# Kernel optimization log

Hardware: AMD Instinct MI355X
Metric: run time of the kernel (lower is better)

The kernel has to match this reference:

```python
import math
import jax, jax.numpy as jnp
import numpy as np

NUM_HEADS = 16
NUM_BUCKETS = 32


def _relative_position_bucket(relative_position):
    # Faithful to the torch code: only n = -(mem - ctx) >= 0 gets nonzero buckets.
    num_buckets = NUM_BUCKETS
    n = jnp.maximum(-relative_position, 0)
    max_exact = num_buckets // 2
    is_small = n < max_exact
    # clamp inside log to avoid log(0); masked out by is_small anyway
    n_safe = jnp.maximum(n, 1).astype(jnp.float32)
    val_if_large = max_exact + (
        jnp.log(n_safe / max_exact) / math.log(num_buckets / max_exact) * (num_buckets - max_exact)
    ).astype(jnp.int32)
    val_if_large = jnp.minimum(val_if_large, num_buckets - 1)
    return jnp.where(is_small, n, val_if_large)


def setup_inputs() -> dict:
    key = jax.random.key(0)
    ks = jax.random.split(key, 8)
    B, S, D = 2, 2048, 1024
    s = 1.0 / math.sqrt(D)
    return {
        "hidden_states": jax.random.normal(ks[0], (B, S, D), jnp.float32),
        "Wq": jax.random.normal(ks[1], (D, D), jnp.float32) * s,
        "bq": jnp.zeros((D,), jnp.float32),
        "Wk": jax.random.normal(ks[2], (D, D), jnp.float32) * s,
        "bk": jnp.zeros((D,), jnp.float32),
        "Wv": jax.random.normal(ks[3], (D, D), jnp.float32) * s,
        "bv": jnp.zeros((D,), jnp.float32),
        "rel_bias": jax.random.normal(ks[4], (NUM_BUCKETS, NUM_HEADS), jnp.float32) * 0.02,
    }


def reference(hidden_states, Wq, bq, Wk, bk, Wv, bv, rel_bias):
    B, S, D = hidden_states.shape
    H = NUM_HEADS
    dh = D // H
    q = (hidden_states @ Wq + bq).reshape(B, S, H, dh)
    k = (hidden_states @ Wk + bk).reshape(B, S, H, dh)
    v = (hidden_states @ Wv + bv).reshape(B, S, H, dh)
    # scores: [B,H,S,S]
    scores = jnp.einsum("bqhd,bkhd->bhqk", q, k) / math.sqrt(dh)
    # T5 relative position bias
    ctx_pos = jnp.arange(S)[:, None]
    mem_pos = jnp.arange(S)[None, :]
    buckets = _relative_position_bucket(mem_pos - ctx_pos)  # [S,S]
    bias = rel_bias[buckets]                                 # [S,S,H]
    bias = jnp.transpose(bias, (2, 0, 1))                    # [H,S,S]
    scores = scores + bias[None]
    attn = jax.nn.softmax(scores, axis=-1)
    context = jnp.einsum("bhqk,bkhd->bqhd", attn, v).reshape(B, S, D)
    return context
```

## Files before the change

### kernel.cpp

```cpp
#include <hip/hip_runtime.h>
#include <hip/hip_bf16.h>

typedef __attribute__((ext_vector_type(8))) short bf16x8;
typedef __attribute__((ext_vector_type(4))) float f32x4;

#define MFMA16x16x32(a, b, c) __builtin_amdgcn_mfma_f32_16x16x32_bf16(a, b, c, 0, 0, 0)
#define EXP2F(x) __builtin_amdgcn_exp2f(x)

#define LOG2E 1.44269504f
#define QSCALE (0.125f * 1.44269504f)

__device__ __forceinline__ unsigned short f2b(float x) {
    union { float f; unsigned int u; } v; v.f = x;
    unsigned int r = v.u + 0x7FFFu + ((v.u >> 16) & 1u);
    return (unsigned short)(r >> 16);
}

__device__ __forceinline__ unsigned pkbf2(float a, float b) {
    float2 f; f.x = a; f.y = b;
    __hip_bfloat162 h = __float22bfloat162_rn(f);
    union { __hip_bfloat162 h2; unsigned u; } cv; cv.h2 = h;
    return cv.u;
}

__device__ __forceinline__ void gload_lds16(const unsigned short* g, unsigned short* l) {
    __builtin_amdgcn_global_load_lds((const __attribute__((address_space(1))) void*)g,
                                     (__attribute__((address_space(3))) void*)l, 16, 0, 0);
}

__device__ __forceinline__ f32x4 fmax4(f32x4 a, f32x4 b) {
    f32x4 r;
    r[0] = fmaxf(a[0], b[0]); r[1] = fmaxf(a[1], b[1]);
    r[2] = fmaxf(a[2], b[2]); r[3] = fmaxf(a[3], b[3]);
    return r;
}

__global__ __launch_bounds__(256) void prep_kernel(const float* __restrict__ hidden,
                                                   const float* __restrict__ Wq,
                                                   const float* __restrict__ Wk,
                                                   const float* __restrict__ Wv,
                                                   const float* __restrict__ rel_bias,
                                                   unsigned short* __restrict__ hA,
                                                   unsigned short* __restrict__ WTall,
                                                   float* __restrict__ bt) {
    int blk = blockIdx.x;
    int t = threadIdx.x;
    if (blk < 3072) {
        int z = blk >> 10;
        int xy = blk & 1023;
        int bx = xy & 31, by = xy >> 5;
        const float* in = (z == 0) ? Wq : (z == 1) ? Wk : Wv;
        unsigned short* outp = WTall + (size_t)z * 1024 * 1024;
        __shared__ float tile[32][33];
        int tx = t & 31, ty = t >> 5;
        int x = bx * 32 + tx;
        int y0 = by * 32;
        #pragma unroll
        for (int j = ty; j < 32; j += 8)
            tile[j][tx] = in[(size_t)(y0 + j) * 1024 + x];
        __syncthreads();
        int ox = y0 + tx;
        int oy0 = bx * 32;
        #pragma unroll
        for (int j = ty; j < 32; j += 8)
            outp[(size_t)(oy0 + j) * 1024 + ox] = f2b(tile[tx][j]);
    } else if (blk < 7168) {
        int i = ((blk - 3072) * 256 + t) * 4;
        float4 v = *reinterpret_cast<const float4*>(hidden + i);
        ushort4 o;
        o.x = f2b(v.x); o.y = f2b(v.y); o.z = f2b(v.z); o.w = f2b(v.w);
        *reinterpret_cast<ushort4*>(hA + i) = o;
    } else {
        int n = (blk - 7168) * 256 + t;
        int bucket;
        if (n < 16) {
            bucket = n;
        } else {
            float nf = (float)n;
            int v = 16 + (int)((logf(nf / 16.0f) / 0.69314718f) * 16.0f);
            bucket = v < 31 ? v : 31;
        }
        #pragma unroll
        for (int h = 0; h < 16; ++h)
            bt[(size_t)h * 2048 + n] = rel_bias[bucket * 16 + h] * LOG2E;
    }
}

__global__ __launch_bounds__(256) void gemm_qkv_kernel(const unsigned short* __restrict__ A,
                                                       const unsigned short* __restrict__ WTall,
                                                       const float* __restrict__ bq,
                                                       const float* __restrict__ bk,
                                                       const float* __restrict__ bv,
                                                       unsigned short* __restrict__ qws,
                                                       unsigned short* __restrict__ kws,
                                                       unsigned short* __restrict__ vtw) {
    const int K = 1024;
    int p = blockIdx.x;
    int lid = (p & 7) * 96 + (p >> 3);
    int bx = lid & 31;
    int rem = lid >> 5;
    int by = rem & 7;
    int z = rem >> 3;

    const unsigned short* Bm = WTall + (size_t)z * 1024 * 1024;
    const float* bias = (z == 0) ? bq : (z == 1) ? bk : bv;

    __shared__ unsigned short As[128 * 32];
    __shared__ unsigned short Bs[128 * 32];

    int t = threadIdx.x;
    int lane = t & 63, w = t >> 6;
    int wr = w >> 1, wc = w & 1;
    int g = lane >> 4, r = lane & 15;
    int m0 = bx * 128, n0 = by * 128;

    int lrow = lane >> 2;
    int lcol = (lane & 3) * 8;
    const unsigned short* ga0 = A + (size_t)(m0 + w * 32 + lrow) * K + lcol;
    const unsigned short* ga1 = ga0 + 16 * K;
    const unsigned short* gb0 = Bm + (size_t)(n0 + w * 32 + lrow) * K + lcol;
    const unsigned short* gb1 = gb0 + 16 * K;
    unsigned short* lA0 = &As[(w * 32) * 32];
    unsigned short* lA1 = &As[(w * 32 + 16) * 32];
    unsigned short* lB0 = &Bs[(w * 32) * 32];
    unsigned short* lB1 = &Bs[(w * 32 + 16) * 32];

    f32x4 acc[4][4] = {};

    for (int kb = 0; kb < K; kb += 32) {
        gload_lds16(ga0 + kb, lA0);
        gload_lds16(ga1 + kb, lA1);
        gload_lds16(gb0 + kb, lB0);
        gload_lds16(gb1 + kb, lB1);
        __syncthreads();

        bf16x8 af[4], bfr[4];
        #pragma unroll
        for (int i = 0; i < 4; ++i)
            af[i] = *reinterpret_cast<const bf16x8*>(&As[(wr * 64 + i * 16 + r) * 32 + g * 8]);
        #pragma unroll
        for (int j = 0; j < 4; ++j)
            bfr[j] = *reinterpret_cast<const bf16x8*>(&Bs[(wc * 64 + j * 16 + r) * 32 + g * 8]);
        #pragma unroll
        for (int i = 0; i < 4; ++i) {
            #pragma unroll
            for (int j = 0; j < 4; ++j)
                acc[i][j] = MFMA16x16x32(af[i], bfr[j], acc[i][j]);
        }
        __syncthreads();
    }

    if (z < 2) {
        unsigned short* C = (z == 0) ? qws : kws;
        float sc = (z == 0) ? QSCALE : 1.0f;
        #pragma unroll
        for (int j = 0; j < 4; ++j) {
            int n = n0 + wc * 64 + j * 16 + r;
            float bj = bias[n];
            #pragma unroll
            for (int i = 0; i < 4; ++i) {
                int mbase = m0 + wr * 64 + i * 16 + g * 4;
                #pragma unroll
                for (int e = 0; e < 4; ++e)
                    C[(size_t)(mbase + e) * 1024 + n] = f2b((acc[i][j][e] + bj) * sc);
            }
        }
    } else {
        #pragma unroll
        for (int j = 0; j < 4; ++j) {
            int n = n0 + wc * 64 + j * 16 + r;
            int hh = n >> 6, d = n & 63;
            float bj = bias[n];
            #pragma unroll
            for (int i = 0; i < 4; ++i) {
                int mbase = m0 + wr * 64 + i * 16 + g * 4;
                int bb = mbase >> 11;
                int kk5 = mbase & 31;
                int pbase = ((kk5 >> 2) & 3) * 8 + ((kk5 >> 4) & 1) * 4;
                int sp = ((mbase & 2047) & ~31) | pbase;
                ushort4 pk4;
                pk4.x = f2b(acc[i][j][0] + bj);
                pk4.y = f2b(acc[i][j][1] + bj);
                pk4.z = f2b(acc[i][j][2] + bj);
                pk4.w = f2b(acc[i][j][3] + bj);
                *reinterpret_cast<ushort4*>(vtw + ((size_t)((bb * 16 + hh) * 64 + d)) * 2048 + sp) = pk4;
            }
        }
    }
}

__global__ __launch_bounds__(256, 2) void attn_kernel(const unsigned short* __restrict__ qg,
                                                      const unsigned short* __restrict__ kg,
                                                      const unsigned short* __restrict__ vt,
                                                      const float* __restrict__ bt,
                                                      float* __restrict__ out) {
    int p = blockIdx.x;
    int lid = (p & 7) * 64 + (p >> 3);
    int bh = lid >> 4, qt = lid & 15;
    int b = bh >> 4, h = bh & 15;
    int t = threadIdx.x;
    int lane = t & 63, w = t >> 6;
    int g = lane >> 4, r = lane & 15;

    __shared__ unsigned short Ks[2][64][72];
    __shared__ unsigned short Vs[2][64][72];
    __shared__ float bts[256];

    bts[t] = bt[(size_t)h * 2048 + t];

    int q0 = qt * 128 + w * 32 + r;
    int q1 = q0 + 16;
    const unsigned short* qp0 = qg + ((size_t)(b * 2048 + q0)) * 1024 + h * 64;
    const unsigned short* qp1 = qg + ((size_t)(b * 2048 + q1)) * 1024 + h * 64;
    bf16x8 qa0 = *reinterpret_cast<const bf16x8*>(qp0 + g * 8);
    bf16x8 qb0 = *reinterpret_cast<const bf16x8*>(qp0 + 32 + g * 8);
    bf16x8 qa1 = *reinterpret_cast<const bf16x8*>(qp1 + g * 8);
    bf16x8 qb1 = *reinterpret_cast<const bf16x8*>(qp1 + 32 + g * 8);

    bf16x8 vones;
    #pragma unroll
    for (int j = 0; j < 8; ++j) vones[j] = (short)0x3F80;

    int srow = t >> 3;
    int sce = (t & 7) * 8;
    const unsigned short* kgp = kg + (size_t)(b * 2048 + srow) * 1024 + h * 64 + sce;
    const unsigned short* vgp = vt + ((size_t)(b * 16 + h) * 64 + srow) * 2048 + sce;

    {
        bf16x8 a0 = *reinterpret_cast<const bf16x8*>(kgp);
        bf16x8 a1 = *reinterpret_cast<const bf16x8*>(kgp + 32 * 1024);
        bf16x8 b0 = *reinterpret_cast<const bf16x8*>(vgp);
        bf16x8 b1 = *reinterpret_cast<const bf16x8*>(vgp + 32 * 2048);
        *reinterpret_cast<bf16x8*>(&Ks[0][srow][sce]) = a0;
        *reinterpret_cast<bf16x8*>(&Ks[0][srow + 32][sce]) = a1;
        *reinterpret_cast<bf16x8*>(&Vs[0][srow][sce]) = b0;
        *reinterpret_cast<bf16x8*>(&Vs[0][srow + 32][sce]) = b1;
    }
    kgp += 64 * 1024;
    vgp += 64;
    __syncthreads();

    float b0c = bts[0];
    float b31c = bts[31];

    float mr0 = -1e30f, mr1 = -1e30f;
    f32x4 o0[4] = {}, o1[4] = {};
    f32x4 d0 = {}, d1 = {};

    #pragma unroll 2
    for (int kvi = 0; kvi < 32; ++kvi) {
        int kv = kvi * 64;
        int cur = kvi & 1;
        bool hasnext = kvi < 31;
        bf16x8 nk0, nk1, nv0, nv1;
        if (hasnext) {
            nk0 = *reinterpret_cast<const bf16x8*>(kgp);
            nk1 = *reinterpret_cast<const bf16x8*>(kgp + 32 * 1024);
            nv0 = *reinterpret_cast<const bf16x8*>(vgp);
            nv1 = *reinterpret_cast<const bf16x8*>(vgp + 32 * 2048);
            kgp += 64 * 1024;
            vgp += 64;
        }

        f32x4 sc0[4], sc1[4];
        __builtin_amdgcn_s_setprio(1);
        #pragma unroll
        for (int kt = 0; kt < 4; ++kt) {
            bf16x8 ka = *reinterpret_cast<const bf16x8*>(&Ks[cur][kt * 16 + r][g * 8]);
            bf16x8 kb2 = *reinterpret_cast<const bf16x8*>(&Ks[cur][kt * 16 + r][32 + g * 8]);
            f32x4 s0 = {}; s0 = MFMA16x16x32(ka, qa0, s0); sc0[kt] = MFMA16x16x32(kb2, qb0, s0);
            f32x4 s1 = {}; s1 = MFMA16x16x32(ka, qa1, s1); sc1[kt] = MFMA16x16x32(kb2, qb1, s1);
        }
        __builtin_amdgcn_s_setprio(0);

        int dd = 2 * qt - kvi;
        bool slow = (dd >= -1) && (dd <= 1);
        float cb = slow ? 0.f : (dd >= 2 ? b31c : b0c);
        if (slow) {
            #pragma unroll
            for (int kt = 0; kt < 4; ++kt) {
                int nb0 = q0 - (kv + kt * 16 + g * 4);
                int nb1 = nb0 + 16;
                #pragma unroll
                for (int e = 0; e < 4; ++e) {
                    int n0i = nb0 - e; n0i = n0i < 0 ? 0 : n0i;
                    int n1i = nb1 - e; n1i = n1i < 0 ? 0 : n1i;
                    sc0[kt][e] += bts[n0i];
                    sc1[kt][e] += bts[n1i];
                }
            }
        }

        union { unsigned u[8]; bf16x8 v2[2]; } pk0, pk1;
        {
            f32x4 mx = fmax4(fmax4(sc0[0], sc0[1]), fmax4(sc0[2], sc0[3]));
            float pmax = fmaxf(fmaxf(mx[0], mx[1]), fmaxf(mx[2], mx[3]));
            pmax = fmaxf(pmax, __shfl_xor(pmax, 16));
            pmax = fmaxf(pmax, __shfl_xor(pmax, 32));
            float pb = pmax + cb;
            if (!__all(pb - mr0 <= 8.0f)) {
                float mnew = fmaxf(mr0, pb);
                float scale = EXP2F(mr0 - mnew);
                float s0 = __shfl(scale, g * 4 + 0);
                float s1 = __shfl(scale, g * 4 + 1);
                float s2 = __shfl(scale, g * 4 + 2);
                float s3 = __shfl(scale, g * 4 + 3);
                #pragma unroll
                for (int nt = 0; nt < 4; ++nt) {
                    o0[nt][0] *= s0; o0[nt][1] *= s1; o0[nt][2] *= s2; o0[nt][3] *= s3;
                }
                d0[0] *= s0; d0[1] *= s1; d0[2] *= s2; d0[3] *= s3;
                mr0 = mnew;
            }
            float moff = mr0 - cb;
            #pragma unroll
            for (int kt = 0; kt < 4; ++kt) {
                float p0 = EXP2F(sc0[kt][0] - moff);
                float p1 = EXP2F(sc0[kt][1] - moff);
                float p2 = EXP2F(sc0[kt][2] - moff);
                float p3 = EXP2F(sc0[kt][3] - moff);
                pk0.u[kt * 2 + 0] = pkbf2(p0, p1);
                pk0.u[kt * 2 + 1] = pkbf2(p2, p3);
            }
        }
        {
            f32x4 mx = fmax4(fmax4(sc1[0], sc1[1]), fmax4(sc1[2], sc1[3]));
            float pmax = fmaxf(fmaxf(mx[0], mx[1]), fmaxf(mx[2], mx[3]));
            pmax = fmaxf(pmax, __shfl_xor(pmax, 16));
            pmax = fmaxf(pmax, __shfl_xor(pmax, 32));
            float pb = pmax + cb;
            if (!__all(pb - mr1 <= 8.0f)) {
                float mnew = fmaxf(mr1, pb);
                float scale = EXP2F(mr1 - mnew);
                float s0 = __shfl(scale, g * 4 + 0);
                float s1 = __shfl(scale, g * 4 + 1);
                float s2 = __shfl(scale, g * 4 + 2);
                float s3 = __shfl(scale, g * 4 + 3);
                #pragma unroll
                for (int nt = 0; nt < 4; ++nt) {
                    o1[nt][0] *= s0; o1[nt][1] *= s1; o1[nt][2] *= s2; o1[nt][3] *= s3;
                }
                d1[0] *= s0; d1[1] *= s1; d1[2] *= s2; d1[3] *= s3;
                mr1 = mnew;
            }
            float moff = mr1 - cb;
            #pragma unroll
            for (int kt = 0; kt < 4; ++kt) {
                float p0 = EXP2F(sc1[kt][0] - moff);
                float p1 = EXP2F(sc1[kt][1] - moff);
                float p2 = EXP2F(sc1[kt][2] - moff);
                float p3 = EXP2F(sc1[kt][3] - moff);
                pk1.u[kt * 2 + 0] = pkbf2(p0, p1);
                pk1.u[kt * 2 + 1] = pkbf2(p2, p3);
            }
        }

        if (hasnext) {
            *reinterpret_cast<bf16x8*>(&Ks[cur ^ 1][srow][sce]) = nk0;
            *reinterpret_cast<bf16x8*>(&Ks[cur ^ 1][srow + 32][sce]) = nk1;
            *reinterpret_cast<bf16x8*>(&Vs[cur ^ 1][srow][sce]) = nv0;
            *reinterpret_cast<bf16x8*>(&Vs[cur ^ 1][srow + 32][sce]) = nv1;
        }

        __builtin_amdgcn_s_setprio(1);
        #pragma unroll
        for (int c = 0; c < 2; ++c) {
            bf16x8 pf0 = pk0.v2[c];
            bf16x8 pf1 = pk1.v2[c];
            bf16x8 vf0 = *reinterpret_cast<const bf16x8*>(&Vs[cur][0 * 16 + r][c * 32 + g * 8]);
            bf16x8 vf1 = *reinterpret_cast<const bf16x8*>(&Vs[cur][1 * 16 + r][c * 32 + g * 8]);
            bf16x8 vf2 = *reinterpret_cast<const bf16x8*>(&Vs[cur][2 * 16 + r][c * 32 + g * 8]);
            bf16x8 vf3 = *reinterpret_cast<const bf16x8*>(&Vs[cur][3 * 16 + r][c * 32 + g * 8]);
            o0[0] = MFMA16x16x32(pf0, vf0, o0[0]);
            o1[0] = MFMA16x16x32(pf1, vf0, o1[0]);
            o0[1] = MFMA16x16x32(pf0, vf1, o0[1]);
            o1[1] = MFMA16x16x32(pf1, vf1, o1[1]);
            o0[2] = MFMA16x16x32(pf0, vf2, o0[2]);
            o1[2] = MFMA16x16x32(pf1, vf2, o1[2]);
            o0[3] = MFMA16x16x32(pf0, vf3, o0[3]);
            o1[3] = MFMA16x16x32(pf1, vf3, o1[3]);
            d0 = MFMA16x16x32(pf0, vones, d0);
            d1 = MFMA16x16x32(pf1, vones, d1);
        }
        __builtin_amdgcn_s_setprio(0);

        __syncthreads();
    }

    #pragma unroll
    for (int e = 0; e < 4; ++e) {
        int qr0 = qt * 128 + w * 32 + g * 4 + e;
        float inv0 = 1.0f / d0[e];
        size_t ob0 = ((size_t)(b * 2048 + qr0)) * 1024 + h * 64 + r;
        float inv1 = 1.0f / d1[e];
        size_t ob1 = ob0 + (size_t)16 * 1024;
        #pragma unroll
        for (int nt = 0; nt < 4; ++nt) {
            out[ob0 + nt * 16] = o0[nt][e] * inv0;
            out[ob1 + nt * 16] = o1[nt][e] * inv1;
        }
    }
}

extern "C" void kernel_launch(void* const* d_in, const int* in_sizes, int n_in,
                              void* d_out, int out_size, void* d_ws, size_t ws_size,
                              hipStream_t stream) {
    const float* hidden = (const float*)d_in[0];
    const float* Wq = (const float*)d_in[1];
    const float* bq = (const float*)d_in[2];
    const float* Wk = (const float*)d_in[3];
    const float* bk = (const float*)d_in[4];
    const float* Wv = (const float*)d_in[5];
    const float* bv = (const float*)d_in[6];
    const float* rel_bias = (const float*)d_in[7];
    float* out = (float*)d_out;

    char* ws = (char*)d_ws;
    unsigned short* WT  = (unsigned short*)(ws);
    unsigned short* qws = (unsigned short*)(ws + (size_t)6 * 1024 * 1024);
    unsigned short* kws = (unsigned short*)(ws + (size_t)14 * 1024 * 1024);
    unsigned short* vtw = (unsigned short*)(ws + (size_t)22 * 1024 * 1024);
    float* bt           = (float*)(ws + (size_t)38 * 1024 * 1024);
    unsigned short* hA  = (unsigned short*)d_out;

    prep_kernel<<<7176, 256, 0, stream>>>(hidden, Wq, Wk, Wv, rel_bias, hA, WT, bt);
    gemm_qkv_kernel<<<768, 256, 0, stream>>>(hA, WT, bq, bk, bv, qws, kws, vtw);
    attn_kernel<<<512, 256, 0, stream>>>(qws, kws, vtw, bt, out);
}
```

Baseline: 193.2 us.

## Double K-step in QKV GEMM and widen attention KV tile to 128

The QKV GEMM now stages 64-wide K slices in shared memory per iteration and processes them as two MFMA halves, which halves the number of barriers. It also sets an occupancy hint of 3 blocks per CU. The attention kernel moves from 64-key to 128-key KV tiles, which halves loop iterations, softmax max reductions and barriers, and adjusts the near-diagonal slow-path condition to match. In exchange, shared memory use and register pressure both rise: score and packed-probability arrays double in size. That could cut occupancy below the 2-block launch bound or cause spills.

```diff
diff --git a/kernel.cpp b/kernel.cpp
--- a/kernel.cpp
+++ b/kernel.cpp
@@ -86,14 +86,14 @@
     }
 }
 
-__global__ __launch_bounds__(256) void gemm_qkv_kernel(const unsigned short* __restrict__ A,
-                                                       const unsigned short* __restrict__ WTall,
-                                                       const float* __restrict__ bq,
-                                                       const float* __restrict__ bk,
-                                                       const float* __restrict__ bv,
-                                                       unsigned short* __restrict__ qws,
-                                                       unsigned short* __restrict__ kws,
-                                                       unsigned short* __restrict__ vtw) {
+__global__ __launch_bounds__(256, 3) void gemm_qkv_kernel(const unsigned short* __restrict__ A,
+                                                          const unsigned short* __restrict__ WTall,
+                                                          const float* __restrict__ bq,
+                                                          const float* __restrict__ bk,
+                                                          const float* __restrict__ bv,
+                                                          unsigned short* __restrict__ qws,
+                                                          unsigned short* __restrict__ kws,
+                                                          unsigned short* __restrict__ vtw) {
     const int K = 1024;
     int p = blockIdx.x;
     int lid = (p & 7) * 96 + (p >> 3);
@@ -105,8 +105,8 @@
     const unsigned short* Bm = WTall + (size_t)z * 1024 * 1024;
     const float* bias = (z == 0) ? bq : (z == 1) ? bk : bv;
 
-    __shared__ unsigned short As[128 * 32];
-    __shared__ unsigned short Bs[128 * 32];
+    __shared__ unsigned short As[128 * 64];
+    __shared__ unsigned short Bs[128 * 64];
 
     int t = threadIdx.x;
     int lane = t & 63, w = t >> 6;
@@ -114,38 +114,38 @@
     int g = lane >> 4, r = lane & 15;
     int m0 = bx * 128, n0 = by * 128;
 
-    int lrow = lane >> 2;
-    int lcol = (lane & 3) * 8;
-    const unsigned short* ga0 = A + (size_t)(m0 + w * 32 + lrow) * K + lcol;
-    const unsigned short* ga1 = ga0 + 16 * K;
-    const unsigned short* gb0 = Bm + (size_t)(n0 + w * 32 + lrow) * K + lcol;
-    const unsigned short* gb1 = gb0 + 16 * K;
-    unsigned short* lA0 = &As[(w * 32) * 32];
-    unsigned short* lA1 = &As[(w * 32 + 16) * 32];
-    unsigned short* lB0 = &Bs[(w * 32) * 32];
-    unsigned short* lB1 = &Bs[(w * 32 + 16) * 32];
+    int lrow = lane >> 3;
+    int lcol = (lane & 7) * 8;
+    const unsigned short* ga = A + (size_t)(m0 + w * 32 + lrow) * K + lcol;
+    const unsigned short* gb = Bm + (size_t)(n0 + w * 32 + lrow) * K + lcol;
+    unsigned short* lA = &As[(w * 32) * 64];
+    unsigned short* lB = &Bs[(w * 32) * 64];
 
     f32x4 acc[4][4] = {};
 
-    for (int kb = 0; kb < K; kb += 32) {
-        gload_lds16(ga0 + kb, lA0);
-        gload_lds16(ga1 + kb, lA1);
-        gload_lds16(gb0 + kb, lB0);
-        gload_lds16(gb1 + kb, lB1);
+    for (int kb = 0; kb < K; kb += 64) {
+        #pragma unroll
+        for (int j = 0; j < 4; ++j) {
+            gload_lds16(ga + kb + (size_t)(8 * j) * K, lA + (8 * j) * 64);
+            gload_lds16(gb + kb + (size_t)(8 * j) * K, lB + (8 * j) * 64);
+        }
         __syncthreads();
 
-        bf16x8 af[4], bfr[4];
-        #pragma unroll
-        for (int i = 0; i < 4; ++i)
-            af[i] = *reinterpret_cast<const bf16x8*>(&As[(wr * 64 + i * 16 + r) * 32 + g * 8]);
-        #pragma unroll
-        for (int j = 0; j < 4; ++j)
-            bfr[j] = *reinterpret_cast<const bf16x8*>(&Bs[(wc * 64 + j * 16 + r) * 32 + g * 8]);
-        #pragma unroll
-        for (int i = 0; i < 4; ++i) {
+        #pragma unroll
+        for (int half = 0; half < 2; ++half) {
+            bf16x8 af[4], bfr[4];
+            #pragma unroll
+            for (int i = 0; i < 4; ++i)
+                af[i] = *reinterpret_cast<const bf16x8*>(&As[(wr * 64 + i * 16 + r) * 64 + half * 32 + g * 8]);
             #pragma unroll
             for (int j = 0; j < 4; ++j)
-                acc[i][j] = MFMA16x16x32(af[i], bfr[j], acc[i][j]);
+                bfr[j] = *reinterpret_cast<const bf16x8*>(&Bs[(wc * 64 + j * 16 + r) * 64 + half * 32 + g * 8]);
+            #pragma unroll
+            for (int i = 0; i < 4; ++i) {
+                #pragma unroll
+                for (int j = 0; j < 4; ++j)
+                    acc[i][j] = MFMA16x16x32(af[i], bfr[j], acc[i][j]);
+            }
         }
         __syncthreads();
     }
@@ -202,8 +202,8 @@
     int lane = t & 63, w = t >> 6;
     int g = lane >> 4, r = lane & 15;
 
-    __shared__ unsigned short Ks[2][64][72];
-    __shared__ unsigned short Vs[2][64][72];
+    __shared__ unsigned short Ks[2][128][72];
+    __shared__ unsigned short Vs[2][64][136];
     __shared__ float bts[256];
 
     bts[t] = bt[(size_t)h * 2048 + t];
@@ -224,20 +224,21 @@
     int srow = t >> 3;
     int sce = (t & 7) * 8;
     const unsigned short* kgp = kg + (size_t)(b * 2048 + srow) * 1024 + h * 64 + sce;
-    const unsigned short* vgp = vt + ((size_t)(b * 16 + h) * 64 + srow) * 2048 + sce;
+    int vrow = t >> 2;
+    int vc = (t & 3) * 8;
+    const unsigned short* vgp = vt + ((size_t)(b * 16 + h) * 64 + vrow) * 2048 + vc;
 
     {
-        bf16x8 a0 = *reinterpret_cast<const bf16x8*>(kgp);
-        bf16x8 a1 = *reinterpret_cast<const bf16x8*>(kgp + 32 * 1024);
-        bf16x8 b0 = *reinterpret_cast<const bf16x8*>(vgp);
-        bf16x8 b1 = *reinterpret_cast<const bf16x8*>(vgp + 32 * 2048);
-        *reinterpret_cast<bf16x8*>(&Ks[0][srow][sce]) = a0;
-        *reinterpret_cast<bf16x8*>(&Ks[0][srow + 32][sce]) = a1;
-        *reinterpret_cast<bf16x8*>(&Vs[0][srow][sce]) = b0;
-        *reinterpret_cast<bf16x8*>(&Vs[0][srow + 32][sce]) = b1;
-    }
-    kgp += 64 * 1024;
-    vgp += 64;
+        #pragma unroll
+        for (int j = 0; j < 4; ++j) {
+            bf16x8 a = *reinterpret_cast<const bf16x8*>(kgp + (size_t)(32 * j) * 1024);
+            *reinterpret_cast<bf16x8*>(&Ks[0][srow + 32 * j][sce]) = a;
+            bf16x8 v = *reinterpret_cast<const bf16x8*>(vgp + 32 * j);
+            *reinterpret_cast<bf16x8*>(&Vs[0][vrow][vc + 32 * j]) = v;
+        }
+    }
+    kgp += 128 * 1024;
+    vgp += 128;
     __syncthreads();
 
     float b0c = bts[0];
@@ -248,24 +249,24 @@
     f32x4 d0 = {}, d1 = {};
 
     #pragma unroll 2
-    for (int kvi = 0; kvi < 32; ++kvi) {
-        int kv = kvi * 64;
+    for (int kvi = 0; kvi < 16; ++kvi) {
         int cur = kvi & 1;
-        bool hasnext = kvi < 31;
-        bf16x8 nk0, nk1, nv0, nv1;
+        bool hasnext = kvi < 15;
+        bf16x8 nk[4], nv[4];
         if (hasnext) {
-            nk0 = *reinterpret_cast<const bf16x8*>(kgp);
-            nk1 = *reinterpret_cast<const bf16x8*>(kgp + 32 * 1024);
-            nv0 = *reinterpret_cast<const bf16x8*>(vgp);
-            nv1 = *reinterpret_cast<const bf16x8*>(vgp + 32 * 2048);
-            kgp += 64 * 1024;
-            vgp += 64;
-        }
-
-        f32x4 sc0[4], sc1[4];
+            #pragma unroll
+            for (int j = 0; j < 4; ++j) {
+                nk[j] = *reinterpret_cast<const bf16x8*>(kgp + (size_t)(32 * j) * 1024);
+                nv[j] = *reinterpret_cast<const bf16x8*>(vgp + 32 * j);
+            }
+            kgp += 128 * 1024;
+            vgp += 128;
+        }
+
+        f32x4 sc0[8], sc1[8];
         __builtin_amdgcn_s_setprio(1);
         #pragma unroll
-        for (int kt = 0; kt < 4; ++kt) {
+        for (int kt = 0; kt < 8; ++kt) {
             bf16x8 ka = *reinterpret_cast<const bf16x8*>(&Ks[cur][kt * 16 + r][g * 8]);
             bf16x8 kb2 = *reinterpret_cast<const bf16x8*>(&Ks[cur][kt * 16 + r][32 + g * 8]);
             f32x4 s0 = {}; s0 = MFMA16x16x32(ka, qa0, s0); sc0[kt] = MFMA16x16x32(kb2, qb0, s0);
@@ -273,13 +274,13 @@
         }
         __builtin_amdgcn_s_setprio(0);
 
-        int dd = 2 * qt - kvi;
-        bool slow = (dd >= -1) && (dd <= 1);
+        int dd = qt - kvi;
+        bool slow = (dd == 0) || (dd == 1);
         float cb = slow ? 0.f : (dd >= 2 ? b31c : b0c);
         if (slow) {
             #pragma unroll
-            for (int kt = 0; kt < 4; ++kt) {
-                int nb0 = q0 - (kv + kt * 16 + g * 4);
+            for (int kt = 0; kt < 8; ++kt) {
+                int nb0 = q0 - (kvi * 128 + kt * 16 + g * 4);
                 int nb1 = nb0 + 16;
                 #pragma unroll
                 for (int e = 0; e < 4; ++e) {
@@ -291,9 +292,10 @@
             }
         }
 
-        union { unsigned u[8]; bf16x8 v2[2]; } pk0, pk1;
+        union { unsigned u[16]; bf16x8 v2[4]; } pk0, pk1;
         {
-            f32x4 mx = fmax4(fmax4(sc0[0], sc0[1]), fmax4(sc0[2], sc0[3]));
+            f32x4 mx = fmax4(fmax4(fmax4(sc0[0], sc0[1]), fmax4(sc0[2], sc0[3])),
+                             fmax4(fmax4(sc0[4], sc0[5]), fmax4(sc0[6], sc0[7])));
             float pmax = fmaxf(fmaxf(mx[0], mx[1]), fmaxf(mx[2], mx[3]));
             pmax = fmaxf(pmax, __shfl_xor(pmax, 16));
             pmax = fmaxf(pmax, __shfl_xor(pmax, 32));
@@ -314,7 +316,7 @@
             }
             float moff = mr0 - cb;
             #pragma unroll
-            for (int kt = 0; kt < 4; ++kt) {
+            for (int kt = 0; kt < 8; ++kt) {
                 float p0 = EXP2F(sc0[kt][0] - moff);
                 float p1 = EXP2F(sc0[kt][1] - moff);
                 float p2 = EXP2F(sc0[kt][2] - moff);
@@ -324,7 +326,8 @@
             }
         }
         {
-            f32x4 mx = fmax4(fmax4(sc1[0], sc1[1]), fmax4(sc1[2], sc1[3]));
+            f32x4 mx = fmax4(fmax4(fmax4(sc1[0], sc1[1]), fmax4(sc1[2], sc1[3])),
+                             fmax4(fmax4(sc1[4], sc1[5]), fmax4(sc1[6], sc1[7])));
             float pmax = fmaxf(fmaxf(mx[0], mx[1]), fmaxf(mx[2], mx[3]));
             pmax = fmaxf(pmax, __shfl_xor(pmax, 16));
             pmax = fmaxf(pmax, __shfl_xor(pmax, 32));
@@ -345,7 +348,7 @@
             }
             float moff = mr1 - cb;
             #pragma unroll
-            for (int kt = 0; kt < 4; ++kt) {
+            for (int kt = 0; kt < 8; ++kt) {
                 float p0 = EXP2F(sc1[kt][0] - moff);
                 float p1 = EXP2F(sc1[kt][1] - moff);
                 float p2 = EXP2F(sc1[kt][2] - moff);
@@ -356,15 +359,16 @@
         }
 
         if (hasnext) {
-            *reinterpret_cast<bf16x8*>(&Ks[cur ^ 1][srow][sce]) = nk0;
-            *reinterpret_cast<bf16x8*>(&Ks[cur ^ 1][srow + 32][sce]) = nk1;
-            *reinterpret_cast<bf16x8*>(&Vs[cur ^ 1][srow][sce]) = nv0;
-            *reinterpret_cast<bf16x8*>(&Vs[cur ^ 1][srow + 32][sce]) = nv1;
+            #pragma unroll
+            for (int j = 0; j < 4; ++j) {
+                *reinterpret_cast<bf16x8*>(&Ks[cur ^ 1][srow + 32 * j][sce]) = nk[j];
+                *reinterpret_cast<bf16x8*>(&Vs[cur ^ 1][vrow][vc + 32 * j]) = nv[j];
+            }
         }
 
         __builtin_amdgcn_s_setprio(1);
         #pragma unroll
-        for (int c = 0; c < 2; ++c) {
+        for (int c = 0; c < 4; ++c) {
             bf16x8 pf0 = pk0.v2[c];
             bf16x8 pf1 = pk1.v2[c];
             bf16x8 vf0 = *reinterpret_cast<const bf16x8*>(&Vs[cur][0 * 16 + r][c * 32 + g * 8]);
```

Measured after the change: 175.0 us. -9.4%, faster.
